# Performance work log

Hardware: AMD Instinct MI355X
Metric: run time of the kernel (lower is better)

## Reference

```python
import jax, jax.numpy as jnp
import numpy as np

EMBED_DIM = 768
HEAD_DIM = 64
BATCH = 8
SEQ = 4096


def setup_inputs() -> dict:
    key = jax.random.key(0)
    k_x, k_q, k_k, k_v = jax.random.split(key, 4)
    input_ids = jax.random.normal(k_x, (BATCH, SEQ, EMBED_DIM), dtype=jnp.float32)
    # nn.Linear(embed, head, bias=False): weight shape [head, embed]; y = x @ W.T
    scale = 1.0 / np.sqrt(EMBED_DIM)
    Wq = jax.random.normal(k_q, (HEAD_DIM, EMBED_DIM), dtype=jnp.float32) * scale
    Wk = jax.random.normal(k_k, (HEAD_DIM, EMBED_DIM), dtype=jnp.float32) * scale
    Wv = jax.random.normal(k_v, (HEAD_DIM, EMBED_DIM), dtype=jnp.float32) * scale
    return {"input_ids": input_ids, "Wq": Wq, "Wk": Wk, "Wv": Wv}


def reference(input_ids, Wq, Wk, Wv):
    # Projections. NOTE: the original module (faithfully reproduced) computes
    # v with q_net, so Wv is unused in the forward math.
    q = jnp.einsum('bse,he->bsh', input_ids, Wq)  # [B,S,H]
    k = jnp.einsum('bse,he->bsh', input_ids, Wk)  # [B,S,H]
    v = jnp.einsum('bse,he->bsh', input_ids, Wq)  # bug in source: uses q_net
    seq_len = q.shape[1]
    # Non-standard scaling: divide by sqrt(seq_len), not sqrt(head_dim)
    scores = jnp.einsum('bqh,bkh->bqk', q, k) / jnp.sqrt(jnp.float32(seq_len))
    # Non-standard softmax axis: over the query axis (dim=1)
    attn_weights = jax.nn.softmax(scores, axis=1)  # [B,Sq,Sk]
    return jnp.einsum('bqk,bkh->bqh', attn_weights, v)
```

## Files before the change

kernel.cpp:

```cpp
#include <hip/hip_runtime.h>
#include <hip/hip_bf16.h>
#include <cstdint>


#define BATCH 8
#define SEQ   4096
#define EMB   768
#define HD    64
#define NROW  (BATCH*SEQ)

#define QSCALE 0.1803368801111201f
#define KSCALE 0.125f
#define CSCALE 5.545177444479562f

typedef float  f32x4  __attribute__((ext_vector_type(4)));
typedef float  f32x16 __attribute__((ext_vector_type(16)));
typedef __bf16 bf16x8 __attribute__((ext_vector_type(8)));
typedef unsigned short u16x8_t __attribute__((ext_vector_type(8)));
typedef unsigned int   u32x4_t __attribute__((ext_vector_type(4)));

__device__ __forceinline__ f32x4 mfma16(bf16x8 a, bf16x8 b, f32x4 c) {
  return __builtin_amdgcn_mfma_f32_16x16x32_bf16(a, b, c, 0, 0, 0);
}
__device__ __forceinline__ f32x16 mfma32(bf16x8 a, bf16x8 b, f32x16 c) {
  return __builtin_amdgcn_mfma_f32_32x32x16_bf16(a, b, c, 0, 0, 0);
}
__device__ __forceinline__ unsigned short f2b(float f) {
  __bf16 h = (__bf16)f;
  return __builtin_bit_cast(unsigned short, h);
}
__device__ __forceinline__ float b2f(unsigned short u) {
  unsigned int x = ((unsigned int)u) << 16;
  return __builtin_bit_cast(float, x);
}
__device__ __forceinline__ bf16x8 ldsA(const unsigned short* p) {
  return __builtin_bit_cast(bf16x8, *(const u16x8_t*)p);
}
__device__ __forceinline__ float expf2(float x) {
  float r; asm("v_exp_f32 %0, %1" : "=v"(r) : "v"(x)); return r;
}
__device__ __forceinline__ unsigned cvtpk(float lo, float hi) {
  unsigned r; asm("v_cvt_pk_bf16_f32 %0, %1, %2" : "=v"(r) : "v"(lo), "v"(hi)); return r;
}
__device__ __forceinline__ void plane32swap(unsigned &a, unsigned &b) {
  asm volatile("v_permlane32_swap_b32 %0, %1" : "+v"(a), "+v"(b));
}
__device__ __forceinline__ void glld16(const void* g, void* l) {
  __builtin_amdgcn_global_load_lds(
      (const __attribute__((address_space(1))) void*)g,
      (__attribute__((address_space(3))) void*)l, 16, 0, 0);
}
__device__ __forceinline__ int sidx(int r, int h) {
  return r * 64 + (h ^ ((r & 7) << 3));
}

__global__ __launch_bounds__(256) void wcvt_kernel(
    const float* __restrict__ Wq, const float* __restrict__ Wk,
    unsigned short* __restrict__ Wb) {
  int ci = blockIdx.x * 256 + threadIdx.x;
  int r = ci / 96, c8 = ci % 96;
  const float* src = (r < 64 ? Wq + (size_t)r * EMB : Wk + (size_t)(r - 64) * EMB) + c8 * 8;
  float4 a = *(const float4*)src, d = *(const float4*)(src + 4);
  u16x8_t o;
  o[0]=f2b(a.x); o[1]=f2b(a.y); o[2]=f2b(a.z); o[3]=f2b(a.w);
  o[4]=f2b(d.x); o[5]=f2b(d.y); o[6]=f2b(d.z); o[7]=f2b(d.w);
  *(u16x8_t*)(Wb + (size_t)ci * 8) = o;
}

__global__ __launch_bounds__(256) void proj_kernel(
    const float* __restrict__ X, const unsigned short* __restrict__ Wb,
    unsigned short* __restrict__ Qb, unsigned short* __restrict__ Kb) {
  __shared__ unsigned short Ws[2][8192];
  const int t = threadIdx.x, lane = t & 63, w = t >> 6;
  const int c = lane & 15, g = lane >> 4;
  const int row0 = blockIdx.x * 64;
  f32x4 acc[8];
#pragma unroll
  for (int f = 0; f < 8; ++f) { acc[f][0]=0.f; acc[f][1]=0.f; acc[f][2]=0.f; acc[f][3]=0.f; }

  auto STAGE = [&](int ec, int bb) {
#pragma unroll
    for (int i = 0; i < 4; ++i) {
      int rr = w + 4 * i;
      int ci = rr * 64 + lane;
      int r = ci >> 3, cL = ci & 7;
      glld16(Wb + (size_t)r * EMB + ec * 64 + (cL ^ (r & 7)) * 8, (void*)&Ws[bb][rr * 512]);
    }
  };
  STAGE(0, 0);
  __syncthreads();
  for (int ec = 0; ec < 12; ++ec) {
    if (ec < 11) STAGE(ec + 1, (ec + 1) & 1);
    bf16x8 Af[2];
#pragma unroll
    for (int es = 0; es < 2; ++es) {
      const float* xp = X + (size_t)(row0 + 16 * w + c) * EMB + ec * 64 + es * 32 + 8 * g;
      float4 v0 = *(const float4*)xp, v1 = *(const float4*)(xp + 4);
      u16x8_t tmp;
      tmp[0]=f2b(v0.x); tmp[1]=f2b(v0.y); tmp[2]=f2b(v0.z); tmp[3]=f2b(v0.w);
      tmp[4]=f2b(v1.x); tmp[5]=f2b(v1.y); tmp[6]=f2b(v1.z); tmp[7]=f2b(v1.w);
      Af[es] = __builtin_bit_cast(bf16x8, tmp);
    }
    const unsigned short* Wt = Ws[ec & 1];
#pragma unroll
    for (int es = 0; es < 2; ++es)
#pragma unroll
      for (int f = 0; f < 8; ++f) {
        bf16x8 Bf = ldsA(&Wt[sidx(16 * f + c, es * 32 + 8 * g)]);
        acc[f] = mfma16(Af[es], Bf, acc[f]);
      }
    __syncthreads();
  }
#pragma unroll
  for (int f = 0; f < 8; ++f) {
    int n = 16 * f + c;
    float sc = (n < 64) ? QSCALE : KSCALE;
#pragma unroll
    for (int r = 0; r < 4; ++r) {
      int ROW = row0 + 16 * w + 4 * g + r;
      unsigned short bv = f2b(acc[f][r] * sc);
      if (n < 64) Qb[(size_t)ROW * 64 + n] = bv;
      else        Kb[(size_t)ROW * 64 + (n - 64)] = bv;
    }
  }
}

__global__ __launch_bounds__(256) void colsum_kernel(
    const unsigned short* __restrict__ Qb, const unsigned short* __restrict__ Kb,
    float* __restrict__ Zpart) {
  __shared__ unsigned short Qs[2][8192];
  const int t = threadIdx.x, lane = t & 63, w = t >> 6;
  const int c = lane & 31, hi = lane >> 5;
  int fid = blockIdx.x + 32 * (blockIdx.y + 4 * blockIdx.z);
  int s = (fid & 7) * 128 + (fid >> 3);
  const int kt = s & 31, qs = (s >> 5) & 3, b = s >> 7;
  const size_t kbase = (size_t)b * SEQ + kt * 128;
  const size_t qbase0 = (size_t)b * SEQ + qs * 1024;

  bf16x8 Kf[4];
#pragma unroll
  for (int es = 0; es < 4; ++es)
    Kf[es] = __builtin_bit_cast(bf16x8,
        *(const u16x8_t*)(Kb + (kbase + 32 * w + c) * 64 + 16 * es + 8 * hi));

  auto STAGE = [&](int qi, int bb) {
#pragma unroll
    for (int i = 0; i < 4; ++i) {
      int rr = w + 4 * i;
      int ci = rr * 64 + lane;
      int r = ci >> 3, cL = ci & 7;
      glld16(Qb + (qbase0 + qi * 128 + r) * 64 + (cL ^ (r & 7)) * 8, (void*)&Qs[bb][rr * 512]);
    }
  };
  float csum = 0.f;
  STAGE(0, 0);
  __syncthreads();
  for (int qi = 0; qi < 8; ++qi) {
    if (qi < 7) STAGE(qi + 1, (qi + 1) & 1);
    const unsigned short* Qt = Qs[qi & 1];
#pragma unroll
    for (int sq = 0; sq < 4; ++sq) {
      f32x16 sv;
#pragma unroll
      for (int i = 0; i < 16; ++i) sv[i] = 0.f;
#pragma unroll
      for (int es = 0; es < 4; ++es) {
        bf16x8 A = ldsA(&Qt[sidx(32 * sq + c, 16 * es + 8 * hi)]);
        sv = mfma32(A, Kf[es], sv);
      }
#pragma unroll
      for (int i = 0; i < 16; ++i) csum += expf2(sv[i]);
    }
    __syncthreads();
  }
  csum += __shfl_xor(csum, 32);
  if (lane < 32)
    Zpart[(kbase + 32 * w + lane) * 4 + qs] = csum;
}

__global__ __launch_bounds__(256) void reduce_c_kernel(
    const float* __restrict__ Zpart, float* __restrict__ cv) {
  int i = blockIdx.x * 256 + threadIdx.x;
  if (i < NROW)
    cv[i] = CSCALE / (Zpart[4*i] + Zpart[4*i+1] + Zpart[4*i+2] + Zpart[4*i+3]);
}

__global__ __launch_bounds__(256) void vtrans_kernel(
    const unsigned short* __restrict__ Qb, const float* __restrict__ cv,
    unsigned short* __restrict__ VT) {
  __shared__ unsigned short T[128 * 72];
  __shared__ float cvs[128];
  const int t = threadIdx.x;
  const int kt = blockIdx.x, b = blockIdx.y;
  const size_t kbase = (size_t)b * SEQ + kt * 128;
#pragma unroll
  for (int it = 0; it < 4; ++it) {
    int ci = t + 256 * it;
    int r = ci >> 3, ch = ci & 7;
    u16x8_t v = *(const u16x8_t*)(Qb + (kbase + r) * 64 + 8 * ch);
    *(u16x8_t*)(&T[r * 72 + 8 * (ch ^ ((r >> 3) & 7))]) = v;
  }
  if (t < 128) cvs[t] = cv[kbase + t];
  __syncthreads();
#pragma unroll
  for (int it = 0; it < 4; ++it) {
    int ci = t + 256 * it;
    int h = ci >> 4, c16 = ci & 15;
    u16x8_t o;
#pragma unroll
    for (int j = 0; j < 8; ++j) {
      int r = 8 * c16 + j;
      unsigned short raw = T[r * 72 + 8 * ((h >> 3) ^ (c16 & 7)) + (h & 7)];
      o[j] = f2b(cvs[r] * b2f(raw));
    }
    *(u16x8_t*)(VT + ((size_t)(b * 64 + h)) * SEQ + kt * 128 + 8 * c16) = o;
  }
}

__global__ __launch_bounds__(256) void attn_kernel(
    const unsigned short* __restrict__ Qb, const unsigned short* __restrict__ Kb,
    const unsigned short* __restrict__ VT, float* __restrict__ outp, int nkt) {
  __shared__ unsigned short KV[2][16384];
  const int t = threadIdx.x, lane = t & 63, w = t >> 6;
  const int c = lane & 31, hi = lane >> 5;
  int fid = blockIdx.x + 32 * (blockIdx.y + gridDim.y * blockIdx.z);
  int qt, ks, b;
  if (gridDim.y == 2) {
    int s = (fid & 7) * 64 + (fid >> 3);
    qt = s & 31; ks = (s >> 5) & 1; b = s >> 6;
  } else { qt = blockIdx.x; ks = 0; b = blockIdx.z; }
  const size_t brow = (size_t)b * SEQ;
  const int q0 = qt * 128;
  const int koff = ks * nkt;

  bf16x8 Qf[4];
#pragma unroll
  for (int es = 0; es < 4; ++es)
    Qf[es] = __builtin_bit_cast(bf16x8,
        *(const u16x8_t*)(Qb + (brow + q0 + 32 * w + c) * 64 + 16 * es + 8 * hi));

  f32x16 acc0, acc1;
#pragma unroll
  for (int i = 0; i < 16; ++i) { acc0[i] = 0.f; acc1[i] = 0.f; }

  auto STAGE = [&](int tt, int bb) {
    const size_t kb0 = brow + (size_t)(koff + tt) * 128;
#pragma unroll
    for (int i = 0; i < 8; ++i) {
      int rr = w + 4 * i;
      int ci = rr * 64 + lane;
      if (rr < 16) {
        int r = ci >> 3, cL = ci & 7;
        glld16(Kb + (kb0 + r) * 64 + (cL ^ (r & 7)) * 8, (void*)&KV[bb][rr * 512]);
      } else {
        int j = ci - 1024;
        int h = j >> 4, cL = j & 15;
        glld16(VT + ((size_t)(b * 64 + h)) * SEQ + (size_t)(koff + tt) * 128 +
                   (cL ^ (h & 7)) * 8,
               (void*)&KV[bb][rr * 512]);
      }
    }
  };

  auto COMPUTE = [&](int bb) {
    const unsigned short* Ks = &KV[bb][0];
    const unsigned short* Vs = &KV[bb][8192];
#pragma unroll
    for (int kb = 0; kb < 4; ++kb) {
      f32x16 sv;
#pragma unroll
      for (int i = 0; i < 16; ++i) sv[i] = 0.f;
#pragma unroll
      for (int es = 0; es < 4; ++es) {
        bf16x8 KA = ldsA(&Ks[sidx(32 * kb + c, 16 * es + 8 * hi)]);
        sv = mfma32(KA, Qf[es], sv);
      }
      float p[16];
#pragma unroll
      for (int i = 0; i < 16; ++i) p[i] = expf2(sv[i]);
      unsigned X0 = cvtpk(p[0], p[1]),  X1 = cvtpk(p[2], p[3]);
      unsigned Y0 = cvtpk(p[4], p[5]),  Y1 = cvtpk(p[6], p[7]);
      plane32swap(X0, Y0); plane32swap(X1, Y1);
      u32x4_t F0 = {X0, X1, Y0, Y1};
      unsigned Z0 = cvtpk(p[8], p[9]),  Z1 = cvtpk(p[10], p[11]);
      unsigned W0 = cvtpk(p[12], p[13]), W1 = cvtpk(p[14], p[15]);
      plane32swap(Z0, W0); plane32swap(Z1, W1);
      u32x4_t F1 = {Z0, Z1, W0, W1};
      bf16x8 fA0 = __builtin_bit_cast(bf16x8, F0);
      bf16x8 fA1 = __builtin_bit_cast(bf16x8, F1);
#pragma unroll
      for (int hb = 0; hb < 2; ++hb) {
        int h = 32 * hb + c;
        int col0 = 32 * kb + 8 * hi;
        bf16x8 VB0 = ldsA(&Vs[h * 128 + (col0 ^ ((h & 7) << 3))]);
        bf16x8 VB1 = ldsA(&Vs[h * 128 + ((col0 + 16) ^ ((h & 7) << 3))]);
        if (hb == 0) { acc0 = mfma32(fA0, VB0, acc0); acc0 = mfma32(fA1, VB1, acc0); }
        else         { acc1 = mfma32(fA0, VB0, acc1); acc1 = mfma32(fA1, VB1, acc1); }
      }
    }
  };

  STAGE(0, 0);
  __syncthreads();
  for (int tt = 0; tt < nkt; ++tt) {
    if (tt + 1 < nkt) STAGE(tt + 1, (tt + 1) & 1);
    COMPUTE(tt & 1);
    __syncthreads();
  }
  float* op = outp + (size_t)ks * NROW * 64;
#pragma unroll
  for (int hb = 0; hb < 2; ++hb)
#pragma unroll
    for (int r = 0; r < 16; ++r) {
      int qrow = (r & 3) + 8 * (r >> 2) + 4 * hi;
      float v = hb ? acc1[r] : acc0[r];
      op[(brow + q0 + 32 * w + qrow) * 64 + 32 * hb + c] = v;
    }
}

__global__ __launch_bounds__(256) void osum_kernel(
    const float4* __restrict__ A, const float4* __restrict__ B,
    float4* __restrict__ O) {
  int i = blockIdx.x * 256 + threadIdx.x;
  float4 x = A[i], y = B[i];
  float4 o; o.x = x.x + y.x; o.y = x.y + y.y; o.z = x.z + y.z; o.w = x.w + y.w;
  O[i] = o;
}

extern "C" void kernel_launch(void* const* d_in, const int* in_sizes, int n_in,
                              void* d_out, int out_size, void* d_ws, size_t ws_size,
                              hipStream_t stream) {
  const float* X  = (const float*)d_in[0];
  const float* Wq = (const float*)d_in[1];
  const float* Wk = (const float*)d_in[2];
  float* Out = (float*)d_out;

  unsigned char* wsb = (unsigned char*)d_ws;
  const size_t QB_OFF = 0;
  const size_t KB_OFF = 4194304;
  const size_t WB_OFF = 8388608;
  const size_t Z_OFF  = 8585216;
  const size_t CV_OFF = 9109504;
  const size_t VT_OFF = 9240576;
  const size_t OP_OFF = 13434880;
  const size_t TOTAL_SPLIT = 30212096;

  unsigned short* Qb = (unsigned short*)(wsb + QB_OFF);
  unsigned short* Kb = (unsigned short*)(wsb + KB_OFF);
  unsigned short* Wb = (unsigned short*)(wsb + WB_OFF);
  float* Zpart       = (float*)(wsb + Z_OFF);
  float* cv          = (float*)(wsb + CV_OFF);
  unsigned short* VT = (unsigned short*)(wsb + VT_OFF);
  float* Opart       = (float*)(wsb + OP_OFF);

  const bool split = (ws_size >= TOTAL_SPLIT);

  hipLaunchKernelGGL(wcvt_kernel, dim3(48), dim3(256), 0, stream, Wq, Wk, Wb);
  hipLaunchKernelGGL(proj_kernel, dim3(NROW / 64), dim3(256), 0, stream, X, Wb, Qb, Kb);
  hipLaunchKernelGGL(colsum_kernel, dim3(32, 4, 8), dim3(256), 0, stream, Qb, Kb, Zpart);
  hipLaunchKernelGGL(reduce_c_kernel, dim3(128), dim3(256), 0, stream, Zpart, cv);
  hipLaunchKernelGGL(vtrans_kernel, dim3(32, 8), dim3(256), 0, stream, Qb, cv, VT);
  if (split) {
    hipLaunchKernelGGL(attn_kernel, dim3(32, 2, 8), dim3(256), 0, stream,
                       Qb, Kb, VT, Opart, 16);
    hipLaunchKernelGGL(osum_kernel, dim3(2048), dim3(256), 0, stream,
                       (const float4*)Opart, (const float4*)(Opart + (size_t)NROW * 64),
                       (float4*)Out);
  } else {
    hipLaunchKernelGGL(attn_kernel, dim3(32, 1, 8), dim3(256), 0, stream,
                       Qb, Kb, VT, Out, 32);
  }
}
```

Baseline: 110.2 us.

## Register-block two 32-row tiles per wave in colsum and attention, fold reduce into vtrans

Each wave in colsum_kernel and attn_kernel now handles two 32-row fragments, so every LDS-loaded Q or K/V fragment feeds twice as many MFMAs. This cuts LDS traffic per unit of work at the cost of more registers. The attention key dimension is split four ways instead of two, and osum sums four partial outputs. The separate reduce_c kernel is removed and its normalization is computed inside vtrans_kernel from Zpart, saving one launch. The larger partial-output workspace may exceed the available size, which would fall back to a 128-block unsplit attention launch with low occupancy.

Result: faster. 105.5 us (-4.3%).

```diff
diff --git a/kernel.cpp b/kernel.cpp
--- a/kernel.cpp
+++ b/kernel.cpp
@@ -131,17 +131,19 @@
   __shared__ unsigned short Qs[2][8192];
   const int t = threadIdx.x, lane = t & 63, w = t >> 6;
   const int c = lane & 31, hi = lane >> 5;
-  int fid = blockIdx.x + 32 * (blockIdx.y + 4 * blockIdx.z);
-  int s = (fid & 7) * 128 + (fid >> 3);
-  const int kt = s & 31, qs = (s >> 5) & 3, b = s >> 7;
-  const size_t kbase = (size_t)b * SEQ + kt * 128;
+  const int fid = blockIdx.x;
+  const int b = fid & 7, rem = fid >> 3;
+  const int kt = rem & 15, qs = rem >> 4;
+  const size_t kbase = (size_t)b * SEQ + kt * 256;
   const size_t qbase0 = (size_t)b * SEQ + qs * 1024;
 
-  bf16x8 Kf[4];
-#pragma unroll
-  for (int es = 0; es < 4; ++es)
-    Kf[es] = __builtin_bit_cast(bf16x8,
-        *(const u16x8_t*)(Kb + (kbase + 32 * w + c) * 64 + 16 * es + 8 * hi));
+  bf16x8 Kf[2][4];
+#pragma unroll
+  for (int j = 0; j < 2; ++j)
+#pragma unroll
+    for (int es = 0; es < 4; ++es)
+      Kf[j][es] = __builtin_bit_cast(bf16x8,
+          *(const u16x8_t*)(Kb + (kbase + 64 * w + 32 * j + c) * 64 + 16 * es + 8 * hi));
 
   auto STAGE = [&](int qi, int bb) {
 #pragma unroll
@@ -152,7 +154,7 @@
       glld16(Qb + (qbase0 + qi * 128 + r) * 64 + (cL ^ (r & 7)) * 8, (void*)&Qs[bb][rr * 512]);
     }
   };
-  float csum = 0.f;
+  float csum[2] = {0.f, 0.f};
   STAGE(0, 0);
   __syncthreads();
   for (int qi = 0; qi < 8; ++qi) {
@@ -160,33 +162,33 @@
     const unsigned short* Qt = Qs[qi & 1];
 #pragma unroll
     for (int sq = 0; sq < 4; ++sq) {
-      f32x16 sv;
-#pragma unroll
-      for (int i = 0; i < 16; ++i) sv[i] = 0.f;
-#pragma unroll
-      for (int es = 0; es < 4; ++es) {
-        bf16x8 A = ldsA(&Qt[sidx(32 * sq + c, 16 * es + 8 * hi)]);
-        sv = mfma32(A, Kf[es], sv);
-      }
-#pragma unroll
-      for (int i = 0; i < 16; ++i) csum += expf2(sv[i]);
+      bf16x8 A[4];
+#pragma unroll
+      for (int es = 0; es < 4; ++es)
+        A[es] = ldsA(&Qt[sidx(32 * sq + c, 16 * es + 8 * hi)]);
+#pragma unroll
+      for (int j = 0; j < 2; ++j) {
+        f32x16 sv;
+#pragma unroll
+        for (int i = 0; i < 16; ++i) sv[i] = 0.f;
+#pragma unroll
+        for (int es = 0; es < 4; ++es) sv = mfma32(A[es], Kf[j][es], sv);
+#pragma unroll
+        for (int i = 0; i < 16; ++i) csum[j] += expf2(sv[i]);
+      }
     }
     __syncthreads();
   }
-  csum += __shfl_xor(csum, 32);
-  if (lane < 32)
-    Zpart[(kbase + 32 * w + lane) * 4 + qs] = csum;
-}
-
-__global__ __launch_bounds__(256) void reduce_c_kernel(
-    const float* __restrict__ Zpart, float* __restrict__ cv) {
-  int i = blockIdx.x * 256 + threadIdx.x;
-  if (i < NROW)
-    cv[i] = CSCALE / (Zpart[4*i] + Zpart[4*i+1] + Zpart[4*i+2] + Zpart[4*i+3]);
+#pragma unroll
+  for (int j = 0; j < 2; ++j) {
+    float v = csum[j] + __shfl_xor(csum[j], 32);
+    if (lane < 32)
+      Zpart[(kbase + 64 * w + 32 * j + lane) * 4 + qs] = v;
+  }
 }
 
 __global__ __launch_bounds__(256) void vtrans_kernel(
-    const unsigned short* __restrict__ Qb, const float* __restrict__ cv,
+    const unsigned short* __restrict__ Qb, const float* __restrict__ Zpart,
     unsigned short* __restrict__ VT) {
   __shared__ unsigned short T[128 * 72];
   __shared__ float cvs[128];
@@ -200,7 +202,10 @@
     u16x8_t v = *(const u16x8_t*)(Qb + (kbase + r) * 64 + 8 * ch);
     *(u16x8_t*)(&T[r * 72 + 8 * (ch ^ ((r >> 3) & 7))]) = v;
   }
-  if (t < 128) cvs[t] = cv[kbase + t];
+  if (t < 128) {
+    const float* zp = Zpart + (kbase + t) * 4;
+    cvs[t] = CSCALE / (zp[0] + zp[1] + zp[2] + zp[3]);
+  }
   __syncthreads();
 #pragma unroll
   for (int it = 0; it < 4; ++it) {
@@ -223,25 +228,28 @@
   __shared__ unsigned short KV[2][16384];
   const int t = threadIdx.x, lane = t & 63, w = t >> 6;
   const int c = lane & 31, hi = lane >> 5;
-  int fid = blockIdx.x + 32 * (blockIdx.y + gridDim.y * blockIdx.z);
-  int qt, ks, b;
-  if (gridDim.y == 2) {
-    int s = (fid & 7) * 64 + (fid >> 3);
-    qt = s & 31; ks = (s >> 5) & 1; b = s >> 6;
-  } else { qt = blockIdx.x; ks = 0; b = blockIdx.z; }
+  const int fid = blockIdx.x;
+  const int b = fid & 7, rem = fid >> 3;
+  const int qt = rem & 15, ks = rem >> 4;
   const size_t brow = (size_t)b * SEQ;
-  const int q0 = qt * 128;
+  const int q0 = qt * 256;
   const int koff = ks * nkt;
 
-  bf16x8 Qf[4];
-#pragma unroll
-  for (int es = 0; es < 4; ++es)
-    Qf[es] = __builtin_bit_cast(bf16x8,
-        *(const u16x8_t*)(Qb + (brow + q0 + 32 * w + c) * 64 + 16 * es + 8 * hi));
-
-  f32x16 acc0, acc1;
-#pragma unroll
-  for (int i = 0; i < 16; ++i) { acc0[i] = 0.f; acc1[i] = 0.f; }
+  bf16x8 Qf[2][4];
+#pragma unroll
+  for (int j = 0; j < 2; ++j)
+#pragma unroll
+    for (int es = 0; es < 4; ++es)
+      Qf[j][es] = __builtin_bit_cast(bf16x8,
+          *(const u16x8_t*)(Qb + (brow + q0 + 64 * w + 32 * j + c) * 64 + 16 * es + 8 * hi));
+
+  f32x16 acc[2][2];
+#pragma unroll
+  for (int j = 0; j < 2; ++j)
+#pragma unroll
+    for (int hb = 0; hb < 2; ++hb)
+#pragma unroll
+      for (int i = 0; i < 16; ++i) acc[j][hb][i] = 0.f;
 
   auto STAGE = [&](int tt, int bb) {
     const size_t kb0 = brow + (size_t)(koff + tt) * 128;
@@ -253,8 +261,8 @@
         int r = ci >> 3, cL = ci & 7;
         glld16(Kb + (kb0 + r) * 64 + (cL ^ (r & 7)) * 8, (void*)&KV[bb][rr * 512]);
       } else {
-        int j = ci - 1024;
-        int h = j >> 4, cL = j & 15;
+        int jj = ci - 1024;
+        int h = jj >> 4, cL = jj & 15;
         glld16(VT + ((size_t)(b * 64 + h)) * SEQ + (size_t)(koff + tt) * 128 +
                    (cL ^ (h & 7)) * 8,
                (void*)&KV[bb][rr * 512]);
@@ -267,35 +275,42 @@
     const unsigned short* Vs = &KV[bb][8192];
 #pragma unroll
     for (int kb = 0; kb < 4; ++kb) {
-      f32x16 sv;
-#pragma unroll
-      for (int i = 0; i < 16; ++i) sv[i] = 0.f;
-#pragma unroll
-      for (int es = 0; es < 4; ++es) {
-        bf16x8 KA = ldsA(&Ks[sidx(32 * kb + c, 16 * es + 8 * hi)]);
-        sv = mfma32(KA, Qf[es], sv);
-      }
-      float p[16];
-#pragma unroll
-      for (int i = 0; i < 16; ++i) p[i] = expf2(sv[i]);
-      unsigned X0 = cvtpk(p[0], p[1]),  X1 = cvtpk(p[2], p[3]);
-      unsigned Y0 = cvtpk(p[4], p[5]),  Y1 = cvtpk(p[6], p[7]);
-      plane32swap(X0, Y0); plane32swap(X1, Y1);
-      u32x4_t F0 = {X0, X1, Y0, Y1};
-      unsigned Z0 = cvtpk(p[8], p[9]),  Z1 = cvtpk(p[10], p[11]);
-      unsigned W0 = cvtpk(p[12], p[13]), W1 = cvtpk(p[14], p[15]);
-      plane32swap(Z0, W0); plane32swap(Z1, W1);
-      u32x4_t F1 = {Z0, Z1, W0, W1};
-      bf16x8 fA0 = __builtin_bit_cast(bf16x8, F0);
-      bf16x8 fA1 = __builtin_bit_cast(bf16x8, F1);
+      bf16x8 KA[4];
+#pragma unroll
+      for (int es = 0; es < 4; ++es)
+        KA[es] = ldsA(&Ks[sidx(32 * kb + c, 16 * es + 8 * hi)]);
+      bf16x8 fA[2][2];
+#pragma unroll
+      for (int j = 0; j < 2; ++j) {
+        f32x16 sv;
+#pragma unroll
+        for (int i = 0; i < 16; ++i) sv[i] = 0.f;
+#pragma unroll
+        for (int es = 0; es < 4; ++es) sv = mfma32(KA[es], Qf[j][es], sv);
+        float p[16];
+#pragma unroll
+        for (int i = 0; i < 16; ++i) p[i] = expf2(sv[i]);
+        unsigned X0 = cvtpk(p[0], p[1]),  X1 = cvtpk(p[2], p[3]);
+        unsigned Y0 = cvtpk(p[4], p[5]),  Y1 = cvtpk(p[6], p[7]);
+        plane32swap(X0, Y0); plane32swap(X1, Y1);
+        u32x4_t F0 = {X0, X1, Y0, Y1};
+        unsigned Z0 = cvtpk(p[8], p[9]),   Z1 = cvtpk(p[10], p[11]);
+        unsigned W0 = cvtpk(p[12], p[13]), W1 = cvtpk(p[14], p[15]);
+        plane32swap(Z0, W0); plane32swap(Z1, W1);
+        u32x4_t F1 = {Z0, Z1, W0, W1};
+        fA[j][0] = __builtin_bit_cast(bf16x8, F0);
+        fA[j][1] = __builtin_bit_cast(bf16x8, F1);
+      }
 #pragma unroll
       for (int hb = 0; hb < 2; ++hb) {
         int h = 32 * hb + c;
         int col0 = 32 * kb + 8 * hi;
         bf16x8 VB0 = ldsA(&Vs[h * 128 + (col0 ^ ((h & 7) << 3))]);
         bf16x8 VB1 = ldsA(&Vs[h * 128 + ((col0 + 16) ^ ((h & 7) << 3))]);
-        if (hb == 0) { acc0 = mfma32(fA0, VB0, acc0); acc0 = mfma32(fA1, VB1, acc0); }
-        else         { acc1 = mfma32(fA0, VB0, acc1); acc1 = mfma32(fA1, VB1, acc1); }
+        acc[0][hb] = mfma32(fA[0][0], VB0, acc[0][hb]);
+        acc[0][hb] = mfma32(fA[0][1], VB1, acc[0][hb]);
+        acc[1][hb] = mfma32(fA[1][0], VB0, acc[1][hb]);
+        acc[1][hb] = mfma32(fA[1][1], VB1, acc[1][hb]);
       }
     }
   };
@@ -309,21 +324,27 @@
   }
   float* op = outp + (size_t)ks * NROW * 64;
 #pragma unroll
-  for (int hb = 0; hb < 2; ++hb)
-#pragma unroll
-    for (int r = 0; r < 16; ++r) {
-      int qrow = (r & 3) + 8 * (r >> 2) + 4 * hi;
-      float v = hb ? acc1[r] : acc0[r];
-      op[(brow + q0 + 32 * w + qrow) * 64 + 32 * hb + c] = v;
-    }
+  for (int j = 0; j < 2; ++j)
+#pragma unroll
+    for (int hb = 0; hb < 2; ++hb)
+#pragma unroll
+      for (int r = 0; r < 16; ++r) {
+        int qrow = (r & 3) + 8 * (r >> 2) + 4 * hi;
+        op[(brow + q0 + 64 * w + 32 * j + qrow) * 64 + 32 * hb + c] = acc[j][hb][r];
+      }
 }
 
 __global__ __launch_bounds__(256) void osum_kernel(
     const float4* __restrict__ A, const float4* __restrict__ B,
+    const float4* __restrict__ C, const float4* __restrict__ D,
     float4* __restrict__ O) {
   int i = blockIdx.x * 256 + threadIdx.x;
-  float4 x = A[i], y = B[i];
-  float4 o; o.x = x.x + y.x; o.y = x.y + y.y; o.z = x.z + y.z; o.w = x.w + y.w;
+  float4 x = A[i], y = B[i], z = C[i], u = D[i];
+  float4 o;
+  o.x = (x.x + y.x) + (z.x + u.x);
+  o.y = (x.y + y.y) + (z.y + u.y);
+  o.z = (x.z + y.z) + (z.z + u.z);
+  o.w = (x.w + y.w) + (z.w + u.w);
   O[i] = o;
 }
 
@@ -340,16 +361,14 @@
   const size_t KB_OFF = 4194304;
   const size_t WB_OFF = 8388608;
   const size_t Z_OFF  = 8585216;
-  const size_t CV_OFF = 9109504;
   const size_t VT_OFF = 9240576;
   const size_t OP_OFF = 13434880;
-  const size_t TOTAL_SPLIT = 30212096;
+  const size_t TOTAL_SPLIT = OP_OFF + (size_t)4 * NROW * 64 * 4;
 
   unsigned short* Qb = (unsigned short*)(wsb + QB_OFF);
   unsigned short* Kb = (unsigned short*)(wsb + KB_OFF);
   unsigned short* Wb = (unsigned short*)(wsb + WB_OFF);
   float* Zpart       = (float*)(wsb + Z_OFF);
-  float* cv          = (float*)(wsb + CV_OFF);
   unsigned short* VT = (unsigned short*)(wsb + VT_OFF);
   float* Opart       = (float*)(wsb + OP_OFF);
 
@@ -357,17 +376,18 @@
 
   hipLaunchKernelGGL(wcvt_kernel, dim3(48), dim3(256), 0, stream, Wq, Wk, Wb);
   hipLaunchKernelGGL(proj_kernel, dim3(NROW / 64), dim3(256), 0, stream, X, Wb, Qb, Kb);
-  hipLaunchKernelGGL(colsum_kernel, dim3(32, 4, 8), dim3(256), 0, stream, Qb, Kb, Zpart);
-  hipLaunchKernelGGL(reduce_c_kernel, dim3(128), dim3(256), 0, stream, Zpart, cv);
-  hipLaunchKernelGGL(vtrans_kernel, dim3(32, 8), dim3(256), 0, stream, Qb, cv, VT);
+  hipLaunchKernelGGL(colsum_kernel, dim3(512), dim3(256), 0, stream, Qb, Kb, Zpart);
+  hipLaunchKernelGGL(vtrans_kernel, dim3(32, 8), dim3(256), 0, stream, Qb, Zpart, VT);
   if (split) {
-    hipLaunchKernelGGL(attn_kernel, dim3(32, 2, 8), dim3(256), 0, stream,
-                       Qb, Kb, VT, Opart, 16);
+    hipLaunchKernelGGL(attn_kernel, dim3(512), dim3(256), 0, stream,
+                       Qb, Kb, VT, Opart, 8);
+    const size_t PS = (size_t)NROW * 64;
     hipLaunchKernelGGL(osum_kernel, dim3(2048), dim3(256), 0, stream,
-                       (const float4*)Opart, (const float4*)(Opart + (size_t)NROW * 64),
+                       (const float4*)Opart, (const float4*)(Opart + PS),
+                       (const float4*)(Opart + 2 * PS), (const float4*)(Opart + 3 * PS),
                        (float4*)Out);
   } else {
-    hipLaunchKernelGGL(attn_kernel, dim3(32, 1, 8), dim3(256), 0, stream,
+    hipLaunchKernelGGL(attn_kernel, dim3(128), dim3(256), 0, stream,
                        Qb, Kb, VT, Out, 32);
   }
 }
```
